# Kernel tuning notes

Hardware: AMD Instinct MI355X
Metric: run time of the kernel (lower is better)

The kernel has to match this reference:

```python
import jax, jax.numpy as jnp
import numpy as np

N = 50000      # nodes
E = 800000     # edges
G = 2000       # graphs
F_IN = 34
HID = 256
H = 8
D = 32         # HID // H
L = 5


def _layer_norm(x, g, b, eps=1e-5):
    m = x.mean(-1, keepdims=True)
    v = ((x - m) ** 2).mean(-1, keepdims=True)
    return (x - m) / jnp.sqrt(v + eps) * g + b


def _gelu(x):
    return jax.nn.gelu(x, approximate=False)  # torch exact GELU


def _segment_softmax(scores, seg, n):
    # scores: [E', H], seg: [E'] target node ids
    m = jax.ops.segment_max(scores, seg, num_segments=n)
    m = jnp.where(jnp.isfinite(m), m, 0.0)
    ex = jnp.exp(scores - m[seg])
    den = jax.ops.segment_sum(ex, seg, num_segments=n)
    return ex / (den[seg] + 1e-16)


def setup_inputs() -> dict:
    key = jax.random.key(0)
    ks = iter(jax.random.split(key, 64))

    def p(shape, fan):
        return (jax.random.normal(next(ks), shape, jnp.float32) / np.sqrt(fan)).astype(jnp.float32)

    inp = {}
    inp['x'] = jax.random.normal(next(ks), (N, F_IN), jnp.float32)
    inp['edge_index'] = jax.random.randint(next(ks), (2, E), 0, N, jnp.int32)
    inp['batch'] = jnp.sort(jax.random.randint(next(ks), (N,), 0, G, jnp.int32))

    # input embed
    inp['in_W'] = p((F_IN, HID), F_IN); inp['in_b'] = jnp.zeros((HID,), jnp.float32)
    inp['in_ln_g'] = jnp.ones((HID,), jnp.float32); inp['in_ln_b'] = jnp.zeros((HID,), jnp.float32)
    # 5 GATv2 layers (stacked on leading dim)
    inp['gat_Wl'] = p((L, HID, HID), HID); inp['gat_bl'] = jnp.zeros((L, HID), jnp.float32)
    inp['gat_Wr'] = p((L, HID, HID), HID); inp['gat_br'] = jnp.zeros((L, HID), jnp.float32)
    inp['gat_att'] = p((L, H, D), D)
    inp['gat_bias'] = jnp.zeros((L, HID), jnp.float32)
    inp['gat_ln_g'] = jnp.ones((L, HID), jnp.float32); inp['gat_ln_b'] = jnp.zeros((L, HID), jnp.float32)
    # TransformerConv
    inp['tr_Wq'] = p((HID, HID), HID); inp['tr_bq'] = jnp.zeros((HID,), jnp.float32)
    inp['tr_Wk'] = p((HID, HID), HID); inp['tr_bk'] = jnp.zeros((HID,), jnp.float32)
    inp['tr_Wv'] = p((HID, HID), HID); inp['tr_bv'] = jnp.zeros((HID,), jnp.float32)
    inp['tr_Wskip'] = p((HID, HID), HID); inp['tr_bskip'] = jnp.zeros((HID,), jnp.float32)
    inp['tr_ln_g'] = jnp.ones((HID,), jnp.float32); inp['tr_ln_b'] = jnp.zeros((HID,), jnp.float32)
    # output proj
    inp['out_W'] = p((2 * HID, 2 * HID), 2 * HID); inp['out_b'] = jnp.zeros((2 * HID,), jnp.float32)
    inp['out_ln_g'] = jnp.ones((2 * HID,), jnp.float32); inp['out_ln_b'] = jnp.zeros((2 * HID,), jnp.float32)
    return inp


def reference(x, edge_index, batch,
              in_W, in_b, in_ln_g, in_ln_b,
              gat_Wl, gat_bl, gat_Wr, gat_br, gat_att, gat_bias, gat_ln_g, gat_ln_b,
              tr_Wq, tr_bq, tr_Wk, tr_bk, tr_Wv, tr_bv, tr_Wskip, tr_bskip, tr_ln_g, tr_ln_b,
              out_W, out_b, out_ln_g, out_ln_b):
    # input embedding (dropout inactive in eval)
    h = _gelu(_layer_norm(x @ in_W + in_b, in_ln_g, in_ln_b))

    src, dst = edge_index[0], edge_index[1]  # PyG: row=source j, col=target i
    loops = jnp.arange(N, dtype=src.dtype)
    s2 = jnp.concatenate([src, loops])  # GATv2 adds self loops
    d2 = jnp.concatenate([dst, loops])

    for l in range(L):  # small fixed loop over layers
        xl = (h @ gat_Wl[l] + gat_bl[l]).reshape(N, H, D)  # source transform / message
        xr = (h @ gat_Wr[l] + gat_br[l]).reshape(N, H, D)  # target transform
        e = jax.nn.leaky_relu(xl[s2] + xr[d2], 0.2)        # [E', H, D]
        score = jnp.einsum('ehd,hd->eh', e, gat_att[l])
        alpha = _segment_softmax(score, d2, N)             # softmax over incoming edges
        out = jax.ops.segment_sum(xl[s2] * alpha[..., None], d2, num_segments=N)
        out = out.reshape(N, HID) + gat_bias[l]
        h = h + _gelu(_layer_norm(out, gat_ln_g[l], gat_ln_b[l]))

    # TransformerConv (no self loops, root_weight skip connection)
    q = (h @ tr_Wq + tr_bq).reshape(N, H, D)
    k = (h @ tr_Wk + tr_bk).reshape(N, H, D)
    v = (h @ tr_Wv + tr_bv).reshape(N, H, D)
    score = (q[dst] * k[src]).sum(-1) / jnp.sqrt(jnp.float32(D))  # [E, H]
    alpha = _segment_softmax(score, dst, N)
    out = jax.ops.segment_sum(v[src] * alpha[..., None], dst, num_segments=N).reshape(N, HID)
    out = out + h @ tr_Wskip + tr_bskip
    h = h + _layer_norm(out, tr_ln_g, tr_ln_b)

    # global mean + max pool
    cnt = jax.ops.segment_sum(jnp.ones((N,), h.dtype), batch, num_segments=G)
    h_mean = jax.ops.segment_sum(h, batch, num_segments=G) / jnp.maximum(cnt, 1.0)[:, None]
    h_max = jax.ops.segment_max(h, batch, num_segments=G)
    h_max = jnp.where(jnp.isfinite(h_max), h_max, 0.0)
    ge = jnp.concatenate([h_mean, h_max], axis=-1)  # [G, 512]
    return _gelu(_layer_norm(ge @ out_W + out_b, out_ln_g, out_ln_b))
```

## Files before the change

### kernel.cpp

```cpp
#include <hip/hip_runtime.h>
#include <math.h>

#define N_NODES 50000
#define N_EDGES 800000
#define N_GRAPH 2000
#define F_INPUT 34
#define HID 256
#define NLAYER 5

typedef __attribute__((ext_vector_type(8))) short short8;
typedef __attribute__((ext_vector_type(4))) float float4v;

__device__ __forceinline__ float gelu_f(float x) {
  return 0.5f * x * (1.0f + erff(x * 0.70710678118654752440f));
}
__device__ __forceinline__ unsigned short bfr(float f) {
  unsigned u = __float_as_uint(f);
  return (unsigned short)((u + 0x7fffu + ((u >> 16) & 1u)) >> 16);
}
__device__ __forceinline__ float b2f(unsigned short s) {
  return __uint_as_float(((unsigned)s) << 16);
}
__device__ __forceinline__ float4 ld4bf(const unsigned short* p) {
  ushort4 u = *(const ushort4*)p;
  float4 f;
  f.x = b2f(u.x); f.y = b2f(u.y); f.z = b2f(u.z); f.w = b2f(u.w);
  return f;
}

__global__ __launch_bounds__(256) void gemm_bias(
    const float* __restrict__ A, const float* __restrict__ B,
    const float* __restrict__ bias, float* __restrict__ C,
    int M, int Nn, int K, int accum) {
  __shared__ float As[16][64];
  __shared__ float Bs[16][64];
  int tid = threadIdx.x;
  int tx = tid & 15, ty = tid >> 4;
  int row0 = blockIdx.y * 64;
  int col0 = blockIdx.x * 64;
  float acc[4][4] = {};
  int a_r = tid >> 2;
  int a_c = (tid & 3) * 4;
  int b_r = tid >> 4;
  int b_c = (tid & 15) * 4;

  for (int k0 = 0; k0 < K; k0 += 16) {
    int ar = row0 + a_r;
#pragma unroll
    for (int i = 0; i < 4; ++i) {
      int kc = k0 + a_c + i;
      As[a_c + i][a_r] = (ar < M && kc < K) ? A[(long)ar * K + kc] : 0.f;
    }
    int bk = k0 + b_r;
    if (bk < K) {
      float4 bv = *(const float4*)&B[(long)bk * Nn + col0 + b_c];
      Bs[b_r][b_c + 0] = bv.x; Bs[b_r][b_c + 1] = bv.y;
      Bs[b_r][b_c + 2] = bv.z; Bs[b_r][b_c + 3] = bv.w;
    } else {
      Bs[b_r][b_c + 0] = 0.f; Bs[b_r][b_c + 1] = 0.f;
      Bs[b_r][b_c + 2] = 0.f; Bs[b_r][b_c + 3] = 0.f;
    }
    __syncthreads();
#pragma unroll
    for (int kk = 0; kk < 16; ++kk) {
      float4 a = *(const float4*)&As[kk][ty * 4];
      float4 b = *(const float4*)&Bs[kk][tx * 4];
      float av[4] = {a.x, a.y, a.z, a.w};
      float bv[4] = {b.x, b.y, b.z, b.w};
#pragma unroll
      for (int i = 0; i < 4; ++i)
#pragma unroll
        for (int j = 0; j < 4; ++j) acc[i][j] += av[i] * bv[j];
    }
    __syncthreads();
  }
  float4 bi = *(const float4*)&bias[col0 + tx * 4];
  float bia[4] = {bi.x, bi.y, bi.z, bi.w};
#pragma unroll
  for (int i = 0; i < 4; ++i) {
    int r = row0 + ty * 4 + i;
    if (r < M) {
      float4* cp = (float4*)&C[(long)r * Nn + col0 + tx * 4];
      float4 o;
      o.x = acc[i][0] + bia[0]; o.y = acc[i][1] + bia[1];
      o.z = acc[i][2] + bia[2]; o.w = acc[i][3] + bia[3];
      if (accum) {
        float4 old = *cp;
        o.x += old.x; o.y += old.y; o.z += old.z; o.w += old.w;
      }
      *cp = o;
    }
  }
}

__global__ __launch_bounds__(256) void gemm_mfma(
    const unsigned short* __restrict__ A, const unsigned short* __restrict__ Bt,
    const float* __restrict__ bias, void* __restrict__ Cv,
    int M, int Nn, int K, int flags) {
  __shared__ unsigned short smem[10240];
#define AS(r, c) smem[(r) * 40 + (c)]
#define BS(r, c) smem[5120 + (r) * 40 + (c)]
  int tid = threadIdx.x;
  int wave = tid >> 6, lane = tid & 63;
  int row0 = blockIdx.y * 128;
  int col0 = blockIdx.x * 128;
  int wm0 = (wave >> 1) * 64;
  int wn0 = (wave & 1) * 64;
  int lr = tid >> 2;
  int lc = (tid & 3) * 8;
  int q = lane >> 4;
  int ln = lane & 15;

  float4v acc[4][4];
#pragma unroll
  for (int i = 0; i < 4; ++i)
#pragma unroll
    for (int j = 0; j < 4; ++j) acc[i][j] = (float4v)0.f;

  for (int k0 = 0; k0 < K; k0 += 32) {
    int r1 = row0 + lr, r2 = row0 + lr + 64;
    uint4 za = {0u, 0u, 0u, 0u};
    uint4 va = (r1 < M) ? *(const uint4*)&A[(size_t)r1 * K + k0 + lc] : za;
    uint4 vb = (r2 < M) ? *(const uint4*)&A[(size_t)r2 * K + k0 + lc] : za;
    uint4 wa = *(const uint4*)&Bt[(size_t)(col0 + lr) * K + k0 + lc];
    uint4 wb = *(const uint4*)&Bt[(size_t)(col0 + lr + 64) * K + k0 + lc];
    *(uint4*)&AS(lr, lc) = va;
    *(uint4*)&AS(lr + 64, lc) = vb;
    *(uint4*)&BS(lr, lc) = wa;
    *(uint4*)&BS(lr + 64, lc) = wb;
    __syncthreads();
    short8 af[4], bf[4];
#pragma unroll
    for (int i = 0; i < 4; ++i) af[i] = *(const short8*)&AS(wm0 + i * 16 + ln, q * 8);
#pragma unroll
    for (int j = 0; j < 4; ++j) bf[j] = *(const short8*)&BS(wn0 + j * 16 + ln, q * 8);
#pragma unroll
    for (int i = 0; i < 4; ++i)
#pragma unroll
      for (int j = 0; j < 4; ++j)
        acc[i][j] = __builtin_amdgcn_mfma_f32_16x16x32_bf16(af[i], bf[j], acc[i][j], 0, 0, 0);
    __syncthreads();
  }
  int rb = (lane >> 4) * 4;
  if (flags & 2) {
    unsigned short* Cb = (unsigned short*)Cv;
    unsigned short* eb = smem + wave * 2560;
#pragma unroll
    for (int p = 0; p < 2; ++p) {
#pragma unroll
      for (int jj = 0; jj < 2; ++jj) {
        int j = p * 2 + jj;
        float bv = bias[col0 + wn0 + j * 16 + ln];
#pragma unroll
        for (int i = 0; i < 4; ++i)
#pragma unroll
          for (int r = 0; r < 4; ++r)
            eb[(i * 16 + rb + r) * 40 + jj * 16 + ln] = bfr(acc[i][j][r] + bv);
      }
      int grow = row0 + wm0 + lane;
      uint4 w0 = *(uint4*)&eb[lane * 40 + 0];
      uint4 w1 = *(uint4*)&eb[lane * 40 + 8];
      uint4 w2 = *(uint4*)&eb[lane * 40 + 16];
      uint4 w3 = *(uint4*)&eb[lane * 40 + 24];
      if (grow < M) {
        unsigned short* dst = Cb + (size_t)grow * Nn + col0 + wn0 + p * 32;
        *(uint4*)&dst[0] = w0;
        *(uint4*)&dst[8] = w1;
        *(uint4*)&dst[16] = w2;
        *(uint4*)&dst[24] = w3;
      }
    }
  } else {
    float* C = (float*)Cv;
#pragma unroll
    for (int j = 0; j < 4; ++j) {
      int col = col0 + wn0 + j * 16 + ln;
      float bv = bias[col];
#pragma unroll
      for (int i = 0; i < 4; ++i)
#pragma unroll
        for (int r = 0; r < 4; ++r) {
          int row = row0 + wm0 + i * 16 + rb + r;
          if (row < M) {
            float v = acc[i][j][r] + bv;
            if (flags & 1) v += C[(size_t)row * Nn + col];
            C[(size_t)row * Nn + col] = v;
          }
        }
    }
  }
#undef AS
#undef BS
}

__global__ __launch_bounds__(256) void prep_w(
    const float* __restrict__ Wl, const float* __restrict__ Wr,
    const float* __restrict__ Wq, const float* __restrict__ Wk,
    const float* __restrict__ Wv, const float* __restrict__ Wsk,
    unsigned short* __restrict__ out) {
  __shared__ float t[32][33];
  int m = blockIdx.z;
  const float* W = (m < 10) ? (((m & 1) ? Wr : Wl) + (size_t)(m >> 1) * 65536)
                 : (m == 10) ? Wq : (m == 11) ? Wk : (m == 12) ? Wv : Wsk;
  int k0 = blockIdx.y * 32, n0 = blockIdx.x * 32;
  int r = threadIdx.x >> 5, c = threadIdx.x & 31;
  for (int rr = r; rr < 32; rr += 8)
    t[rr][c] = W[(size_t)(k0 + rr) * HID + n0 + c];
  __syncthreads();
  unsigned short* o = out + (size_t)m * 65536;
  for (int rr = r; rr < 32; rr += 8)
    o[(size_t)(n0 + rr) * HID + k0 + c] = bfr(t[c][rr]);
}

__global__ __launch_bounds__(256) void prep_wout(const float* __restrict__ W,
                                                 unsigned short* __restrict__ o) {
  __shared__ float t[32][33];
  int k0 = blockIdx.y * 32, n0 = blockIdx.x * 32;
  int r = threadIdx.x >> 5, c = threadIdx.x & 31;
  for (int rr = r; rr < 32; rr += 8)
    t[rr][c] = W[(size_t)(k0 + rr) * 512 + n0 + c];
  __syncthreads();
  for (int rr = r; rr < 32; rr += 8)
    o[(size_t)(n0 + rr) * 512 + k0 + c] = bfr(t[c][rr]);
}

__global__ __launch_bounds__(256) void prep_bias(
    const float* __restrict__ bl, const float* __restrict__ br,
    const float* __restrict__ bq, const float* __restrict__ bk,
    const float* __restrict__ bv, float* __restrict__ out) {
  int i = blockIdx.x * 256 + threadIdx.x;
  if (i < 2560) {
    int l = i >> 9, c = i & 511;
    out[i] = (c < 256) ? bl[l * 256 + c] : br[l * 256 + (c - 256)];
  } else if (i < 3328) {
    int j = i - 2560;
    out[i] = (j < 256) ? bq[j] : (j < 512) ? bk[j - 256] : bv[j - 512];
  }
}

__global__ __launch_bounds__(256) void ln_act(
    const float* __restrict__ in, const float* __restrict__ gam,
    const float* __restrict__ bet, float* __restrict__ out,
    unsigned short* __restrict__ outb,
    int n_rows, int width, int do_gelu) {
  int wid = blockIdx.x * 4 + (threadIdx.x >> 6);
  int lane = threadIdx.x & 63;
  if (wid >= n_rows) return;
  int chunks = width >> 8;
  float4 v[2];
  float s = 0.f;
  for (int c = 0; c < chunks; ++c) {
    int off = c * 256 + lane * 4;
    float4 t = *(const float4*)&in[(size_t)wid * width + off];
    v[c] = t;
    s += t.x + t.y + t.z + t.w;
  }
  for (int o = 1; o < 64; o <<= 1) s += __shfl_xor(s, o);
  float mean = s / (float)width;
  float vs = 0.f;
  for (int c = 0; c < chunks; ++c) {
    float dx = v[c].x - mean, dy = v[c].y - mean, dz = v[c].z - mean, dw = v[c].w - mean;
    vs += dx * dx + dy * dy + dz * dz + dw * dw;
  }
  for (int o = 1; o < 64; o <<= 1) vs += __shfl_xor(vs, o);
  float inv = rsqrtf(vs / (float)width + 1e-5f);
  for (int c = 0; c < chunks; ++c) {
    int off = c * 256 + lane * 4;
    float4 g4 = *(const float4*)&gam[off];
    float4 b4 = *(const float4*)&bet[off];
    float y[4] = {(v[c].x - mean) * inv * g4.x + b4.x,
                  (v[c].y - mean) * inv * g4.y + b4.y,
                  (v[c].z - mean) * inv * g4.z + b4.z,
                  (v[c].w - mean) * inv * g4.w + b4.w};
    if (do_gelu) {
#pragma unroll
      for (int i = 0; i < 4; ++i) y[i] = gelu_f(y[i]);
    }
    size_t idx = (size_t)wid * width + off;
    float4 o4 = {y[0], y[1], y[2], y[3]};
    *(float4*)&out[idx] = o4;
    if (outb) {
      ushort4 ob = {bfr(y[0]), bfr(y[1]), bfr(y[2]), bfr(y[3])};
      *(ushort4*)&outb[idx] = ob;
    }
  }
}

__global__ __launch_bounds__(256) void edge_count(const int* __restrict__ ei,
                                                  int* __restrict__ counts) {
  int e = blockIdx.x * 256 + threadIdx.x;
  if (e < N_EDGES) atomicAdd(&counts[ei[N_EDGES + e]], 1);
}

__global__ __launch_bounds__(1024) void scan1(const int* __restrict__ counts,
                                              int* __restrict__ indptr,
                                              int* __restrict__ bsums, int n) {
  __shared__ int sm[1024];
  int tid = threadIdx.x;
  int i = blockIdx.x * 1024 + tid;
  int v = (i < n) ? counts[i] : 0;
  sm[tid] = v;
  __syncthreads();
  for (int off = 1; off < 1024; off <<= 1) {
    int t = (tid >= off) ? sm[tid - off] : 0;
    __syncthreads();
    sm[tid] += t;
    __syncthreads();
  }
  if (i < n) indptr[i] = sm[tid] - v;
  if (tid == 1023) bsums[blockIdx.x] = sm[1023];
}

__global__ void scan2(int* __restrict__ bsums, int nb) {
  if (threadIdx.x == 0 && blockIdx.x == 0) {
    int acc = 0;
    for (int i = 0; i < nb; ++i) { int t = bsums[i]; bsums[i] = acc; acc += t; }
  }
}

__global__ __launch_bounds__(256) void scan3(const int* __restrict__ bsums,
                                             int* __restrict__ indptr,
                                             int* __restrict__ cursor, int n) {
  int i = blockIdx.x * 256 + threadIdx.x;
  if (i < n) {
    int v = indptr[i] + bsums[i >> 10];
    indptr[i] = v;
    cursor[i] = v;
  }
  if (i == 0) indptr[n] = N_EDGES;
}

__global__ __launch_bounds__(256) void edge_scatter(const int* __restrict__ ei,
                                                    int* __restrict__ cursor,
                                                    int* __restrict__ esrc) {
  int e = blockIdx.x * 256 + threadIdx.x;
  if (e < N_EDGES) {
    int d = ei[N_EDGES + e];
    int p = atomicAdd(&cursor[d], 1);
    esrc[p] = ei[e];
  }
}

__global__ __launch_bounds__(256) void gat_agg(
    const unsigned short* __restrict__ xlr, const float* __restrict__ att,
    const int* __restrict__ indptr, const int* __restrict__ esrc,
    const float* __restrict__ pre_bias, const float* __restrict__ gam,
    const float* __restrict__ bet, float* __restrict__ h,
    unsigned short* __restrict__ hb) {
  int wid = blockIdx.x * 4 + (threadIdx.x >> 6);
  int lane = threadIdx.x & 63;
  if (wid >= N_NODES) return;
  float4 xri = ld4bf(&xlr[(size_t)wid * 512 + 256 + lane * 4]);
  float4 a4 = *(const float4*)&att[lane * 4];
  int beg = indptr[wid], end = indptr[wid + 1];

  float m, lsum, ax, ay, az, aw;
  {
    float4 f = ld4bf(&xlr[(size_t)wid * 512 + lane * 4]);
    float ex = f.x + xri.x; ex = ex > 0.f ? ex : 0.2f * ex;
    float ey = f.y + xri.y; ey = ey > 0.f ? ey : 0.2f * ey;
    float ez = f.z + xri.z; ez = ez > 0.f ? ez : 0.2f * ez;
    float ew = f.w + xri.w; ew = ew > 0.f ? ew : 0.2f * ew;
    float p = ex * a4.x + ey * a4.y + ez * a4.z + ew * a4.w;
    p += __shfl_xor(p, 1); p += __shfl_xor(p, 2); p += __shfl_xor(p, 4);
    m = p; lsum = 1.f;
    ax = f.x; ay = f.y; az = f.z; aw = f.w;
  }
  int e = beg;
  for (; e + 1 < end; e += 2) {
    int j0 = esrc[e], j1 = esrc[e + 1];
    float4 f0 = ld4bf(&xlr[(size_t)j0 * 512 + lane * 4]);
    float4 f1 = ld4bf(&xlr[(size_t)j1 * 512 + lane * 4]);
    {
      float ex = f0.x + xri.x; ex = ex > 0.f ? ex : 0.2f * ex;
      float ey = f0.y + xri.y; ey = ey > 0.f ? ey : 0.2f * ey;
      float ez = f0.z + xri.z; ez = ez > 0.f ? ez : 0.2f * ez;
      float ew = f0.w + xri.w; ew = ew > 0.f ? ew : 0.2f * ew;
      float p = ex * a4.x + ey * a4.y + ez * a4.z + ew * a4.w;
      p += __shfl_xor(p, 1); p += __shfl_xor(p, 2); p += __shfl_xor(p, 4);
      if (p > m) {
        float f = __expf(m - p);
        ax *= f; ay *= f; az *= f; aw *= f; lsum *= f; m = p;
      }
      float w = __expf(p - m);
      ax += w * f0.x; ay += w * f0.y; az += w * f0.z; aw += w * f0.w;
      lsum += w;
    }
    {
      float ex = f1.x + xri.x; ex = ex > 0.f ? ex : 0.2f * ex;
      float ey = f1.y + xri.y; ey = ey > 0.f ? ey : 0.2f * ey;
      float ez = f1.z + xri.z; ez = ez > 0.f ? ez : 0.2f * ez;
      float ew = f1.w + xri.w; ew = ew > 0.f ? ew : 0.2f * ew;
      float p = ex * a4.x + ey * a4.y + ez * a4.z + ew * a4.w;
      p += __shfl_xor(p, 1); p += __shfl_xor(p, 2); p += __shfl_xor(p, 4);
      if (p > m) {
        float f = __expf(m - p);
        ax *= f; ay *= f; az *= f; aw *= f; lsum *= f; m = p;
      }
      float w = __expf(p - m);
      ax += w * f1.x; ay += w * f1.y; az += w * f1.z; aw += w * f1.w;
      lsum += w;
    }
  }
  if (e < end) {
    int j = esrc[e];
    float4 f = ld4bf(&xlr[(size_t)j * 512 + lane * 4]);
    float ex = f.x + xri.x; ex = ex > 0.f ? ex : 0.2f * ex;
    float ey = f.y + xri.y; ey = ey > 0.f ? ey : 0.2f * ey;
    float ez = f.z + xri.z; ez = ez > 0.f ? ez : 0.2f * ez;
    float ew = f.w + xri.w; ew = ew > 0.f ? ew : 0.2f * ew;
    float p = ex * a4.x + ey * a4.y + ez * a4.z + ew * a4.w;
    p += __shfl_xor(p, 1); p += __shfl_xor(p, 2); p += __shfl_xor(p, 4);
    if (p > m) {
      float f2 = __expf(m - p);
      ax *= f2; ay *= f2; az *= f2; aw *= f2; lsum *= f2; m = p;
    }
    float w = __expf(p - m);
    ax += w * f.x; ay += w * f.y; az += w * f.z; aw += w * f.w;
    lsum += w;
  }
  float inv = 1.f / (lsum + 1e-16f);
  float4 pb = *(const float4*)&pre_bias[lane * 4];
  float y0 = ax * inv + pb.x, y1 = ay * inv + pb.y;
  float y2 = az * inv + pb.z, y3 = aw * inv + pb.w;
  float s = y0 + y1 + y2 + y3;
  for (int o = 1; o < 64; o <<= 1) s += __shfl_xor(s, o);
  float mean = s * (1.f / 256.f);
  float d0 = y0 - mean, d1 = y1 - mean, d2 = y2 - mean, d3 = y3 - mean;
  float vs = d0 * d0 + d1 * d1 + d2 * d2 + d3 * d3;
  for (int o = 1; o < 64; o <<= 1) vs += __shfl_xor(vs, o);
  float inv2 = rsqrtf(vs * (1.f / 256.f) + 1e-5f);
  float4 g4 = *(const float4*)&gam[lane * 4];
  float4 b4 = *(const float4*)&bet[lane * 4];
  y0 = gelu_f(d0 * inv2 * g4.x + b4.x);
  y1 = gelu_f(d1 * inv2 * g4.y + b4.y);
  y2 = gelu_f(d2 * inv2 * g4.z + b4.z);
  y3 = gelu_f(d3 * inv2 * g4.w + b4.w);
  size_t idx = (size_t)wid * HID + lane * 4;
  float4 r4 = *(const float4*)&h[idx];
  y0 += r4.x; y1 += r4.y; y2 += r4.z; y3 += r4.w;
  float4 o4 = {y0, y1, y2, y3};
  *(float4*)&h[idx] = o4;
  ushort4 ob = {bfr(y0), bfr(y1), bfr(y2), bfr(y3)};
  *(ushort4*)&hb[idx] = ob;
}

__global__ __launch_bounds__(256) void tr_agg(
    const unsigned short* __restrict__ qkv, const int* __restrict__ indptr,
    const int* __restrict__ esrc, const float* __restrict__ skip,
    const float* __restrict__ gam, const float* __restrict__ bet,
    float* __restrict__ h) {
  int wid = blockIdx.x * 4 + (threadIdx.x >> 6);
  int lane = threadIdx.x & 63;
  if (wid >= N_NODES) return;
  float4 qi = ld4bf(&qkv[(size_t)wid * 768 + lane * 4]);
  int beg = indptr[wid], end = indptr[wid + 1];
  float m = -INFINITY, lsum = 0.f;
  float ax = 0.f, ay = 0.f, az = 0.f, aw = 0.f;
  const float scale = 0.17677669529663687f;
  int e = beg;
  for (; e + 1 < end; e += 2) {
    int j0 = esrc[e], j1 = esrc[e + 1];
    float4 k0 = ld4bf(&qkv[(size_t)j0 * 768 + 256 + lane * 4]);
    float4 v0 = ld4bf(&qkv[(size_t)j0 * 768 + 512 + lane * 4]);
    float4 k1 = ld4bf(&qkv[(size_t)j1 * 768 + 256 + lane * 4]);
    float4 v1 = ld4bf(&qkv[(size_t)j1 * 768 + 512 + lane * 4]);
    {
      float p = qi.x * k0.x + qi.y * k0.y + qi.z * k0.z + qi.w * k0.w;
      p += __shfl_xor(p, 1); p += __shfl_xor(p, 2); p += __shfl_xor(p, 4);
      float sc = p * scale;
      if (sc > m) {
        float f = __expf(m - sc);
        ax *= f; ay *= f; az *= f; aw *= f; lsum *= f; m = sc;
      }
      float w = __expf(sc - m);
      ax += w * v0.x; ay += w * v0.y; az += w * v0.z; aw += w * v0.w;
      lsum += w;
    }
    {
      float p = qi.x * k1.x + qi.y * k1.y + qi.z * k1.z + qi.w * k1.w;
      p += __shfl_xor(p, 1); p += __shfl_xor(p, 2); p += __shfl_xor(p, 4);
      float sc = p * scale;
      if (sc > m) {
        float f = __expf(m - sc);
        ax *= f; ay *= f; az *= f; aw *= f; lsum *= f; m = sc;
      }
      float w = __expf(sc - m);
      ax += w * v1.x; ay += w * v1.y; az += w * v1.z; aw += w * v1.w;
      lsum += w;
    }
  }
  if (e < end) {
    int j = esrc[e];
    float4 kj = ld4bf(&qkv[(size_t)j * 768 + 256 + lane * 4]);
    float4 vj = ld4bf(&qkv[(size_t)j * 768 + 512 + lane * 4]);
    float p = qi.x * kj.x + qi.y * kj.y + qi.z * kj.z + qi.w * kj.w;
    p += __shfl_xor(p, 1); p += __shfl_xor(p, 2); p += __shfl_xor(p, 4);
    float sc = p * scale;
    if (sc > m) {
      float f = __expf(m - sc);
      ax *= f; ay *= f; az *= f; aw *= f; lsum *= f; m = sc;
    }
    float w = __expf(sc - m);
    ax += w * vj.x; ay += w * vj.y; az += w * vj.z; aw += w * vj.w;
    lsum += w;
  }
  float inv = 1.f / (lsum + 1e-16f);
  size_t idx = (size_t)wid * HID + lane * 4;
  float4 sk = *(const float4*)&skip[idx];
  float y0 = ax * inv + sk.x, y1 = ay * inv + sk.y;
  float y2 = az * inv + sk.z, y3 = aw * inv + sk.w;
  float s = y0 + y1 + y2 + y3;
  for (int o = 1; o < 64; o <<= 1) s += __shfl_xor(s, o);
  float mean = s * (1.f / 256.f);
  float d0 = y0 - mean, d1 = y1 - mean, d2 = y2 - mean, d3 = y3 - mean;
  float vs = d0 * d0 + d1 * d1 + d2 * d2 + d3 * d3;
  for (int o = 1; o < 64; o <<= 1) vs += __shfl_xor(vs, o);
  float inv2 = rsqrtf(vs * (1.f / 256.f) + 1e-5f);
  float4 g4 = *(const float4*)&gam[lane * 4];
  float4 b4 = *(const float4*)&bet[lane * 4];
  float4 r4 = *(const float4*)&h[idx];
  float4 o4;
  o4.x = r4.x + d0 * inv2 * g4.x + b4.x;
  o4.y = r4.y + d1 * inv2 * g4.y + b4.y;
  o4.z = r4.z + d2 * inv2 * g4.z + b4.z;
  o4.w = r4.w + d3 * inv2 * g4.w + b4.w;
  *(float4*)&h[idx] = o4;
}

__global__ __launch_bounds__(256) void graph_bounds(const int* __restrict__ batch,
                                                    int* __restrict__ gptr) {
  int i = blockIdx.x * 256 + threadIdx.x;
  if (i >= N_NODES) return;
  int b0 = batch[i];
  if (i == 0)
    for (int g = 0; g <= b0; ++g) gptr[g] = 0;
  int b1 = (i + 1 < N_NODES) ? batch[i + 1] : N_GRAPH;
  for (int g = b0 + 1; g <= b1; ++g) gptr[g] = i + 1;
}

__global__ __launch_bounds__(256) void pool_seg(
    const float* __restrict__ h, const int* __restrict__ gptr,
    unsigned short* __restrict__ geb) {
  int g = blockIdx.x, c = threadIdx.x;
  int s = gptr[g], e = gptr[g + 1];
  float sum = 0.f, mx = -INFINITY;
  for (int r = s; r < e; ++r) {
    float vv = h[(size_t)r * HID + c];
    sum += vv;
    mx = fmaxf(mx, vv);
  }
  int cnt = e - s;
  geb[(size_t)g * 512 + c] = bfr(sum / (float)max(cnt, 1));
  geb[(size_t)g * 512 + 256 + c] = bfr(cnt ? mx : 0.f);
}

static inline void gemm_launch(const float* A, const float* B, const float* bias,
                               float* C, int M, int Nn, int K, int accum,
                               hipStream_t s) {
  dim3 grid(Nn / 64, (M + 63) / 64);
  gemm_bias<<<grid, 256, 0, s>>>(A, B, bias, C, M, Nn, K, accum);
}
static inline void mfma_launch(const unsigned short* A, const unsigned short* Bt,
                               const float* bias, void* C, int M, int Nn, int K,
                               int flags, hipStream_t s) {
  dim3 grid(Nn / 128, (M + 127) / 128);
  gemm_mfma<<<grid, 256, 0, s>>>(A, Bt, bias, C, M, Nn, K, flags);
}

extern "C" void kernel_launch(void* const* d_in, const int* in_sizes, int n_in,
                              void* d_out, int out_size, void* d_ws, size_t ws_size,
                              hipStream_t stream) {
  const float* x       = (const float*)d_in[0];
  const int*   ei      = (const int*)d_in[1];
  const int*   batch   = (const int*)d_in[2];
  const float* in_W    = (const float*)d_in[3];
  const float* in_b    = (const float*)d_in[4];
  const float* in_ln_g = (const float*)d_in[5];
  const float* in_ln_b = (const float*)d_in[6];
  const float* gat_Wl  = (const float*)d_in[7];
  const float* gat_bl  = (const float*)d_in[8];
  const float* gat_Wr  = (const float*)d_in[9];
  const float* gat_br  = (const float*)d_in[10];
  const float* gat_att = (const float*)d_in[11];
  const float* gat_bias= (const float*)d_in[12];
  const float* gat_ln_g= (const float*)d_in[13];
  const float* gat_ln_b= (const float*)d_in[14];
  const float* tr_Wq   = (const float*)d_in[15];
  const float* tr_bq   = (const float*)d_in[16];
  const float* tr_Wk   = (const float*)d_in[17];
  const float* tr_bk   = (const float*)d_in[18];
  const float* tr_Wv   = (const float*)d_in[19];
  const float* tr_bv   = (const float*)d_in[20];
  const float* tr_Wsk  = (const float*)d_in[21];
  const float* tr_bsk  = (const float*)d_in[22];
  const float* tr_ln_g = (const float*)d_in[23];
  const float* tr_ln_b = (const float*)d_in[24];
  const float* out_W   = (const float*)d_in[25];
  const float* out_b   = (const float*)d_in[26];
  const float* out_ln_g= (const float*)d_in[27];
  const float* out_ln_b= (const float*)d_in[28];

  char* w = (char*)d_ws;
  auto take = [&](size_t bytes) -> char* {
    char* p = w;
    w += (bytes + 255) & ~(size_t)255;
    return p;
  };
  const size_t NB = (size_t)N_NODES * HID * sizeof(float);
  float* h    = (float*)take(NB);
  float* aggO = (float*)take(NB);
  unsigned short* hb  = (unsigned short*)take((size_t)N_NODES * HID * 2);
  unsigned short* xq  = (unsigned short*)take((size_t)N_NODES * 768 * 2);
  unsigned short* wbuf= (unsigned short*)take((size_t)(14 * 65536 + 262144) * 2);
  float* bcat = (float*)take(3328 * sizeof(float));
  int* indptr = (int*)take((N_NODES + 1) * sizeof(int));
  int* cursor = (int*)take(N_NODES * sizeof(int));
  int* counts = (int*)take(N_NODES * sizeof(int));
  int* esrc   = (int*)take(N_EDGES * sizeof(int));
  int* bsums  = (int*)take(64 * sizeof(int));
  char* w2 = (char*)xq;
  auto take2 = [&](size_t bytes) -> char* {
    char* p = w2;
    w2 += (bytes + 255) & ~(size_t)255;
    return p;
  };
  int* gptr = (int*)take2((N_GRAPH + 1) * sizeof(int));
  unsigned short* geb = (unsigned short*)take2((size_t)N_GRAPH * 512 * 2);
  float* tbuf = (float*)take2((size_t)N_GRAPH * 512 * sizeof(float));

  const int EB = (N_EDGES + 255) / 256;
  const int WB = (N_NODES + 3) / 4;
  const int NSB = (N_NODES + 1023) / 1024;

  {
    dim3 g(8, 8, 14);
    prep_w<<<g, 256, 0, stream>>>(gat_Wl, gat_Wr, tr_Wq, tr_Wk, tr_Wv, tr_Wsk, wbuf);
    dim3 g2(16, 16);
    prep_wout<<<g2, 256, 0, stream>>>(out_W, wbuf + (size_t)14 * 65536);
    prep_bias<<<13, 256, 0, stream>>>(gat_bl, gat_br, tr_bq, tr_bk, tr_bv, bcat);
  }

  hipMemsetAsync(counts, 0, N_NODES * sizeof(int), stream);
  edge_count<<<EB, 256, 0, stream>>>(ei, counts);
  scan1<<<NSB, 1024, 0, stream>>>(counts, indptr, bsums, N_NODES);
  scan2<<<1, 64, 0, stream>>>(bsums, NSB);
  scan3<<<(N_NODES + 255) / 256, 256, 0, stream>>>(bsums, indptr, cursor, N_NODES);
  edge_scatter<<<EB, 256, 0, stream>>>(ei, cursor, esrc);

  gemm_launch(x, in_W, in_b, aggO, N_NODES, HID, F_INPUT, 0, stream);
  ln_act<<<WB, 256, 0, stream>>>(aggO, in_ln_g, in_ln_b, h, hb, N_NODES, HID, 1);

  for (int l = 0; l < NLAYER; ++l) {
    mfma_launch(hb, wbuf + (size_t)(2 * l) * 65536, bcat + l * 512, xq,
                N_NODES, 512, HID, 2, stream);
    gat_agg<<<WB, 256, 0, stream>>>(xq, gat_att + l * HID, indptr, esrc,
                                    gat_bias + l * HID, gat_ln_g + l * HID,
                                    gat_ln_b + l * HID, h, hb);
  }

  mfma_launch(hb, wbuf + (size_t)13 * 65536, tr_bsk, aggO,
              N_NODES, HID, HID, 0, stream);
  mfma_launch(hb, wbuf + (size_t)10 * 65536, bcat + 2560, xq,
              N_NODES, 768, HID, 2, stream);
  tr_agg<<<WB, 256, 0, stream>>>(xq, indptr, esrc, aggO, tr_ln_g, tr_ln_b, h);

  graph_bounds<<<(N_NODES + 255) / 256, 256, 0, stream>>>(batch, gptr);
  pool_seg<<<N_GRAPH, 256, 0, stream>>>(h, gptr, geb);

  mfma_launch(geb, wbuf + (size_t)14 * 65536, out_b, tbuf,
              N_GRAPH, 512, 512, 0, stream);
  ln_act<<<(N_GRAPH + 3) / 4, 256, 0, stream>>>(tbuf, out_ln_g, out_ln_b,
                                                (float*)d_out, nullptr,
                                                N_GRAPH, 512, 1);
}
```

Baseline: 1.242 ms.

## Use direct global-to-LDS loads in MFMA GEMM, drop online softmax max tracking, bf16 skip

The MFMA GEMM now stages A and B tiles with global_load_lds builtins into an unpadded LDS layout and clamps out-of-range rows instead of zero-filling them. The GAT and Transformer aggregation kernels replace online-softmax rescaling with a fixed reference (the self-loop score for GAT, zero for Transformer) plus a clamp on the exponent, and the GAT loop is unrolled to four edges. The Transformer skip projection is written and read as bf16 rather than fp32, and the unused accumulate paths are removed. Unpadded LDS rows may cause bank conflicts. The fixed-max softmax with a clamp at 60 can diverge numerically from a true max-subtracted softmax when scores are large, and the skip term loses precision from bf16.

```diff
diff --git a/kernel.cpp b/kernel.cpp
--- a/kernel.cpp
+++ b/kernel.cpp
@@ -27,11 +27,16 @@
   f.x = b2f(u.x); f.y = b2f(u.y); f.z = b2f(u.z); f.w = b2f(u.w);
   return f;
 }
+__device__ __forceinline__ void acp16(const unsigned short* g, unsigned short* l) {
+  __builtin_amdgcn_global_load_lds(
+      (const __attribute__((address_space(1))) void*)g,
+      (__attribute__((address_space(3))) void*)l, 16, 0, 0);
+}
 
 __global__ __launch_bounds__(256) void gemm_bias(
     const float* __restrict__ A, const float* __restrict__ B,
     const float* __restrict__ bias, float* __restrict__ C,
-    int M, int Nn, int K, int accum) {
+    int M, int Nn, int K) {
   __shared__ float As[16][64];
   __shared__ float Bs[16][64];
   int tid = threadIdx.x;
@@ -80,15 +85,10 @@
   for (int i = 0; i < 4; ++i) {
     int r = row0 + ty * 4 + i;
     if (r < M) {
-      float4* cp = (float4*)&C[(long)r * Nn + col0 + tx * 4];
       float4 o;
       o.x = acc[i][0] + bia[0]; o.y = acc[i][1] + bia[1];
       o.z = acc[i][2] + bia[2]; o.w = acc[i][3] + bia[3];
-      if (accum) {
-        float4 old = *cp;
-        o.x += old.x; o.y += old.y; o.z += old.z; o.w += old.w;
-      }
-      *cp = o;
+      *(float4*)&C[(long)r * Nn + col0 + tx * 4] = o;
     }
   }
 }
@@ -97,20 +97,31 @@
     const unsigned short* __restrict__ A, const unsigned short* __restrict__ Bt,
     const float* __restrict__ bias, void* __restrict__ Cv,
     int M, int Nn, int K, int flags) {
-  __shared__ unsigned short smem[10240];
-#define AS(r, c) smem[(r) * 40 + (c)]
-#define BS(r, c) smem[5120 + (r) * 40 + (c)]
+  __shared__ unsigned short smem[12288];
+  unsigned short* As = smem;
+  unsigned short* Bs = smem + 4096;
   int tid = threadIdx.x;
   int wave = tid >> 6, lane = tid & 63;
   int row0 = blockIdx.y * 128;
   int col0 = blockIdx.x * 128;
   int wm0 = (wave >> 1) * 64;
   int wn0 = (wave & 1) * 64;
-  int lr = tid >> 2;
-  int lc = (tid & 3) * 8;
   int q = lane >> 4;
   int ln = lane & 15;
 
+  int srow = wave * 16 + (lane >> 2);
+  int scol = (lane & 3) * 8;
+  int ra0 = min(row0 + srow, M - 1);
+  int ra1 = min(row0 + srow + 64, M - 1);
+  const unsigned short* pa0 = A + (size_t)ra0 * K + scol;
+  const unsigned short* pa1 = A + (size_t)ra1 * K + scol;
+  const unsigned short* pb0 = Bt + (size_t)(col0 + srow) * K + scol;
+  const unsigned short* pb1 = Bt + (size_t)(col0 + srow + 64) * K + scol;
+  unsigned short* la0 = As + wave * 512;
+  unsigned short* la1 = As + wave * 512 + 2048;
+  unsigned short* lb0 = Bs + wave * 512;
+  unsigned short* lb1 = Bs + wave * 512 + 2048;
+
   float4v acc[4][4];
 #pragma unroll
   for (int i = 0; i < 4; ++i)
@@ -118,22 +129,18 @@
     for (int j = 0; j < 4; ++j) acc[i][j] = (float4v)0.f;
 
   for (int k0 = 0; k0 < K; k0 += 32) {
-    int r1 = row0 + lr, r2 = row0 + lr + 64;
-    uint4 za = {0u, 0u, 0u, 0u};
-    uint4 va = (r1 < M) ? *(const uint4*)&A[(size_t)r1 * K + k0 + lc] : za;
-    uint4 vb = (r2 < M) ? *(const uint4*)&A[(size_t)r2 * K + k0 + lc] : za;
-    uint4 wa = *(const uint4*)&Bt[(size_t)(col0 + lr) * K + k0 + lc];
-    uint4 wb = *(const uint4*)&Bt[(size_t)(col0 + lr + 64) * K + k0 + lc];
-    *(uint4*)&AS(lr, lc) = va;
-    *(uint4*)&AS(lr + 64, lc) = vb;
-    *(uint4*)&BS(lr, lc) = wa;
-    *(uint4*)&BS(lr + 64, lc) = wb;
+    acp16(pa0 + k0, la0);
+    acp16(pa1 + k0, la1);
+    acp16(pb0 + k0, lb0);
+    acp16(pb1 + k0, lb1);
     __syncthreads();
     short8 af[4], bf[4];
 #pragma unroll
-    for (int i = 0; i < 4; ++i) af[i] = *(const short8*)&AS(wm0 + i * 16 + ln, q * 8);
-#pragma unroll
-    for (int j = 0; j < 4; ++j) bf[j] = *(const short8*)&BS(wn0 + j * 16 + ln, q * 8);
+    for (int i = 0; i < 4; ++i)
+      af[i] = *(const short8*)&As[(wm0 + i * 16 + ln) * 32 + q * 8];
+#pragma unroll
+    for (int j = 0; j < 4; ++j)
+      bf[j] = *(const short8*)&Bs[(wn0 + j * 16 + ln) * 32 + q * 8];
 #pragma unroll
     for (int i = 0; i < 4; ++i)
 #pragma unroll
@@ -181,16 +188,10 @@
 #pragma unroll
         for (int r = 0; r < 4; ++r) {
           int row = row0 + wm0 + i * 16 + rb + r;
-          if (row < M) {
-            float v = acc[i][j][r] + bv;
-            if (flags & 1) v += C[(size_t)row * Nn + col];
-            C[(size_t)row * Nn + col] = v;
-          }
+          if (row < M) C[(size_t)row * Nn + col] = acc[i][j][r] + bv;
         }
     }
   }
-#undef AS
-#undef BS
 }
 
 __global__ __launch_bounds__(256) void prep_w(
@@ -341,6 +342,19 @@
   }
 }
 
+#define GAT_EDGE(f)                                                        \
+  {                                                                        \
+    float ex = f.x + xri.x; ex = ex > 0.f ? ex : 0.2f * ex;                \
+    float ey = f.y + xri.y; ey = ey > 0.f ? ey : 0.2f * ey;                \
+    float ez = f.z + xri.z; ez = ez > 0.f ? ez : 0.2f * ez;                \
+    float ew = f.w + xri.w; ew = ew > 0.f ? ew : 0.2f * ew;                \
+    float p = ex * a4.x + ey * a4.y + ez * a4.z + ew * a4.w;               \
+    p += __shfl_xor(p, 1); p += __shfl_xor(p, 2); p += __shfl_xor(p, 4);   \
+    float wgt = __expf(fminf(p - m0, 60.f));                               \
+    ax += wgt * f.x; ay += wgt * f.y; az += wgt * f.z; aw += wgt * f.w;    \
+    lsum += wgt;                                                           \
+  }
+
 __global__ __launch_bounds__(256) void gat_agg(
     const unsigned short* __restrict__ xlr, const float* __restrict__ att,
     const int* __restrict__ indptr, const int* __restrict__ esrc,
@@ -354,7 +368,7 @@
   float4 a4 = *(const float4*)&att[lane * 4];
   int beg = indptr[wid], end = indptr[wid + 1];
 
-  float m, lsum, ax, ay, az, aw;
+  float m0, lsum, ax, ay, az, aw;
   {
     float4 f = ld4bf(&xlr[(size_t)wid * 512 + lane * 4]);
     float ex = f.x + xri.x; ex = ex > 0.f ? ex : 0.2f * ex;
@@ -363,61 +377,22 @@
     float ew = f.w + xri.w; ew = ew > 0.f ? ew : 0.2f * ew;
     float p = ex * a4.x + ey * a4.y + ez * a4.z + ew * a4.w;
     p += __shfl_xor(p, 1); p += __shfl_xor(p, 2); p += __shfl_xor(p, 4);
-    m = p; lsum = 1.f;
+    m0 = p; lsum = 1.f;
     ax = f.x; ay = f.y; az = f.z; aw = f.w;
   }
   int e = beg;
-  for (; e + 1 < end; e += 2) {
-    int j0 = esrc[e], j1 = esrc[e + 1];
+  for (; e + 3 < end; e += 4) {
+    int j0 = esrc[e], j1 = esrc[e + 1], j2 = esrc[e + 2], j3 = esrc[e + 3];
     float4 f0 = ld4bf(&xlr[(size_t)j0 * 512 + lane * 4]);
     float4 f1 = ld4bf(&xlr[(size_t)j1 * 512 + lane * 4]);
-    {
-      float ex = f0.x + xri.x; ex = ex > 0.f ? ex : 0.2f * ex;
-      float ey = f0.y + xri.y; ey = ey > 0.f ? ey : 0.2f * ey;
-      float ez = f0.z + xri.z; ez = ez > 0.f ? ez : 0.2f * ez;
-      float ew = f0.w + xri.w; ew = ew > 0.f ? ew : 0.2f * ew;
-      float p = ex * a4.x + ey * a4.y + ez * a4.z + ew * a4.w;
-      p += __shfl_xor(p, 1); p += __shfl_xor(p, 2); p += __shfl_xor(p, 4);
-      if (p > m) {
-        float f = __expf(m - p);
-        ax *= f; ay *= f; az *= f; aw *= f; lsum *= f; m = p;
-      }
-      float w = __expf(p - m);
-      ax += w * f0.x; ay += w * f0.y; az += w * f0.z; aw += w * f0.w;
-      lsum += w;
-    }
-    {
-      float ex = f1.x + xri.x; ex = ex > 0.f ? ex : 0.2f * ex;
-      float ey = f1.y + xri.y; ey = ey > 0.f ? ey : 0.2f * ey;
-      float ez = f1.z + xri.z; ez = ez > 0.f ? ez : 0.2f * ez;
-      float ew = f1.w + xri.w; ew = ew > 0.f ? ew : 0.2f * ew;
-      float p = ex * a4.x + ey * a4.y + ez * a4.z + ew * a4.w;
-      p += __shfl_xor(p, 1); p += __shfl_xor(p, 2); p += __shfl_xor(p, 4);
-      if (p > m) {
-        float f = __expf(m - p);
-        ax *= f; ay *= f; az *= f; aw *= f; lsum *= f; m = p;
-      }
-      float w = __expf(p - m);
-      ax += w * f1.x; ay += w * f1.y; az += w * f1.z; aw += w * f1.w;
-      lsum += w;
-    }
-  }
-  if (e < end) {
+    float4 f2 = ld4bf(&xlr[(size_t)j2 * 512 + lane * 4]);
+    float4 f3 = ld4bf(&xlr[(size_t)j3 * 512 + lane * 4]);
+    GAT_EDGE(f0); GAT_EDGE(f1); GAT_EDGE(f2); GAT_EDGE(f3);
+  }
+  for (; e < end; ++e) {
     int j = esrc[e];
     float4 f = ld4bf(&xlr[(size_t)j * 512 + lane * 4]);
-    float ex = f.x + xri.x; ex = ex > 0.f ? ex : 0.2f * ex;
-    float ey = f.y + xri.y; ey = ey > 0.f ? ey : 0.2f * ey;
-    float ez = f.z + xri.z; ez = ez > 0.f ? ez : 0.2f * ez;
-    float ew = f.w + xri.w; ew = ew > 0.f ? ew : 0.2f * ew;
-    float p = ex * a4.x + ey * a4.y + ez * a4.z + ew * a4.w;
-    p += __shfl_xor(p, 1); p += __shfl_xor(p, 2); p += __shfl_xor(p, 4);
-    if (p > m) {
-      float f2 = __expf(m - p);
-      ax *= f2; ay *= f2; az *= f2; aw *= f2; lsum *= f2; m = p;
-    }
-    float w = __expf(p - m);
-    ax += w * f.x; ay += w * f.y; az += w * f.z; aw += w * f.w;
-    lsum += w;
+    GAT_EDGE(f);
   }
   float inv = 1.f / (lsum + 1e-16f);
   float4 pb = *(const float4*)&pre_bias[lane * 4];
@@ -445,9 +420,18 @@
   *(ushort4*)&hb[idx] = ob;
 }
 
+#define TR_EDGE(kj, vj)                                                    \
+  {                                                                        \
+    float p = qi.x * kj.x + qi.y * kj.y + qi.z * kj.z + qi.w * kj.w;       \
+    p += __shfl_xor(p, 1); p += __shfl_xor(p, 2); p += __shfl_xor(p, 4);   \
+    float wgt = __expf(fminf(p * scale, 60.f));                            \
+    ax += wgt * vj.x; ay += wgt * vj.y; az += wgt * vj.z; aw += wgt * vj.w;\
+    lsum += wgt;                                                           \
+  }
+
 __global__ __launch_bounds__(256) void tr_agg(
     const unsigned short* __restrict__ qkv, const int* __restrict__ indptr,
-    const int* __restrict__ esrc, const float* __restrict__ skip,
+    const int* __restrict__ esrc, const unsigned short* __restrict__ skipb,
     const float* __restrict__ gam, const float* __restrict__ bet,
     float* __restrict__ h) {
   int wid = blockIdx.x * 4 + (threadIdx.x >> 6);
@@ -455,7 +439,7 @@
   if (wid >= N_NODES) return;
   float4 qi = ld4bf(&qkv[(size_t)wid * 768 + lane * 4]);
   int beg = indptr[wid], end = indptr[wid + 1];
-  float m = -INFINITY, lsum = 0.f;
+  float lsum = 0.f;
   float ax = 0.f, ay = 0.f, az = 0.f, aw = 0.f;
   const float scale = 0.17677669529663687f;
   int e = beg;
@@ -465,49 +449,17 @@
     float4 v0 = ld4bf(&qkv[(size_t)j0 * 768 + 512 + lane * 4]);
     float4 k1 = ld4bf(&qkv[(size_t)j1 * 768 + 256 + lane * 4]);
     float4 v1 = ld4bf(&qkv[(size_t)j1 * 768 + 512 + lane * 4]);
-    {
-      float p = qi.x * k0.x + qi.y * k0.y + qi.z * k0.z + qi.w * k0.w;
-      p += __shfl_xor(p, 1); p += __shfl_xor(p, 2); p += __shfl_xor(p, 4);
-      float sc = p * scale;
-      if (sc > m) {
-        float f = __expf(m - sc);
-        ax *= f; ay *= f; az *= f; aw *= f; lsum *= f; m = sc;
-      }
-      float w = __expf(sc - m);
-      ax += w * v0.x; ay += w * v0.y; az += w * v0.z; aw += w * v0.w;
-      lsum += w;
-    }
-    {
-      float p = qi.x * k1.x + qi.y * k1.y + qi.z * k1.z + qi.w * k1.w;
-      p += __shfl_xor(p, 1); p += __shfl_xor(p, 2); p += __shfl_xor(p, 4);
-      float sc = p * scale;
-      if (sc > m) {
-        float f = __expf(m - sc);
-        ax *= f; ay *= f; az *= f; aw *= f; lsum *= f; m = sc;
-      }
-      float w = __expf(sc - m);
-      ax += w * v1.x; ay += w * v1.y; az += w * v1.z; aw += w * v1.w;
-      lsum += w;
-    }
+    TR_EDGE(k0, v0); TR_EDGE(k1, v1);
   }
   if (e < end) {
     int j = esrc[e];
     float4 kj = ld4bf(&qkv[(size_t)j * 768 + 256 + lane * 4]);
     float4 vj = ld4bf(&qkv[(size_t)j * 768 + 512 + lane * 4]);
-    float p = qi.x * kj.x + qi.y * kj.y + qi.z * kj.z + qi.w * kj.w;
-    p += __shfl_xor(p, 1); p += __shfl_xor(p, 2); p += __shfl_xor(p, 4);
-    float sc = p * scale;
-    if (sc > m) {
-      float f = __expf(m - sc);
-      ax *= f; ay *= f; az *= f; aw *= f; lsum *= f; m = sc;
-    }
-    float w = __expf(sc - m);
-    ax += w * vj.x; ay += w * vj.y; az += w * vj.z; aw += w * vj.w;
-    lsum += w;
+    TR_EDGE(kj, vj);
   }
   float inv = 1.f / (lsum + 1e-16f);
   size_t idx = (size_t)wid * HID + lane * 4;
-  float4 sk = *(const float4*)&skip[idx];
+  float4 sk = ld4bf(&skipb[idx]);
   float y0 = ax * inv + sk.x, y1 = ay * inv + sk.y;
   float y2 = az * inv + sk.z, y3 = aw * inv + sk.w;
   float s = y0 + y1 + y2 + y3;
@@ -555,12 +507,6 @@
   geb[(size_t)g * 512 + 256 + c] = bfr(cnt ? mx : 0.f);
 }
 
-static inline void gemm_launch(const float* A, const float* B, const float* bias,
-                               float* C, int M, int Nn, int K, int accum,
-                               hipStream_t s) {
-  dim3 grid(Nn / 64, (M + 63) / 64);
-  gemm_bias<<<grid, 256, 0, s>>>(A, B, bias, C, M, Nn, K, accum);
-}
 static inline void mfma_launch(const unsigned short* A, const unsigned short* Bt,
                                const float* bias, void* C, int M, int Nn, int K,
                                int flags, hipStream_t s) {
@@ -619,6 +565,7 @@
   int* counts = (int*)take(N_NODES * sizeof(int));
   int* esrc   = (int*)take(N_EDGES * sizeof(int));
   int* bsums  = (int*)take(64 * sizeof(int));
+  unsigned short* skipb = (unsigned short*)aggO;
   char* w2 = (char*)xq;
   auto take2 = [&](size_t bytes) -> char* {
     char* p = w2;
@@ -648,7 +595,10 @@
   scan3<<<(N_NODES + 255) / 256, 256, 0, stream>>>(bsums, indptr, cursor, N_NODES);
   edge_scatter<<<EB, 256, 0, stream>>>(ei, cursor, esrc);
 
-  gemm_launch(x, in_W, in_b, aggO, N_NODES, HID, F_INPUT, 0, stream);
+  {
+    dim3 grid(HID / 64, (N_NODES + 63) / 64);
+    gemm_bias<<<grid, 256, 0, stream>>>(x, in_W, in_b, aggO, N_NODES, HID, F_INPUT);
+  }
   ln_act<<<WB, 256, 0, stream>>>(aggO, in_ln_g, in_ln_b, h, hb, N_NODES, HID, 1);
 
   for (int l = 0; l < NLAYER; ++l) {
@@ -659,11 +609,11 @@
                                     gat_ln_b + l * HID, h, hb);
   }
 
-  mfma_launch(hb, wbuf + (size_t)13 * 65536, tr_bsk, aggO,
-              N_NODES, HID, HID, 0, stream);
+  mfma_launch(hb, wbuf + (size_t)13 * 65536, tr_bsk, skipb,
+              N_NODES, HID, HID, 2, stream);
   mfma_launch(hb, wbuf + (size_t)10 * 65536, bcat + 2560, xq,
               N_NODES, 768, HID, 2, stream);
-  tr_agg<<<WB, 256, 0, stream>>>(xq, indptr, esrc, aggO, tr_ln_g, tr_ln_b, h);
+  tr_agg<<<WB, 256, 0, stream>>>(xq, indptr, esrc, skipb, tr_ln_g, tr_ln_b, h);
 
   graph_bounds<<<(N_NODES + 255) / 256, 256, 0, stream>>>(batch, gptr);
   pool_seg<<<N_GRAPH, 256, 0, stream>>>(h, gptr, geb);
```

New measurement: 1.169 ms. 1.06x faster.
